# Kernel tuning notes

Hardware: AMD Instinct MI355X
Metric: run time of the kernel (lower is better)

Reference implementation:

```python
import jax, jax.numpy as jnp
import numpy as np

B, L, D, H = 2, 2048, 1024, 16
DK = D // H


def setup_inputs() -> dict:
    key = jax.random.key(0)
    ks = jax.random.split(key, 11)
    s = 0.02
    return {
        "q": jax.random.normal(ks[0], (B, L, D), jnp.float32),
        "k": jax.random.normal(ks[1], (B, L, D), jnp.float32),
        "v": jax.random.normal(ks[2], (B, L, D), jnp.float32),
        "mask": jnp.ones((B, 1, 1, L), jnp.int32),
        "wq": jax.random.normal(ks[3], (D, D), jnp.float32) * s,
        "bq": jnp.zeros((D,), jnp.float32),
        "wk": jax.random.normal(ks[4], (D, D), jnp.float32) * s,
        "bk": jnp.zeros((D,), jnp.float32),
        "wv": jax.random.normal(ks[5], (D, D), jnp.float32) * s,
        "bv": jnp.zeros((D,), jnp.float32),
        "wo": jax.random.normal(ks[6], (D, D), jnp.float32) * s,
        "bo": jnp.zeros((D,), jnp.float32),
    }


def _split_heads(x):
    # (B, L, D) -> (B, H, L, DK)
    return x.reshape(B, L, H, DK).transpose(0, 2, 1, 3)


def reference(q, k, v, mask, wq, bq, wk, bk, wv, bv, wo, bo):
    query = _split_heads(q @ wq.T + bq)
    key = _split_heads(k @ wk.T + bk)
    value = _split_heads(v @ wv.T + bv)
    scale = 1.0 / jnp.sqrt(jnp.asarray(DK, query.dtype))
    # (B, H, Lq, Lk) materialized scores, as in the original module
    scores = jnp.einsum('bhqd,bhkd->bhqk', query, key) * scale
    scores = jnp.where(mask == 0, jnp.asarray(-1e9, scores.dtype), scores)
    weights = jax.nn.softmax(scores, axis=-1)
    out = jnp.einsum('bhqk,bhkd->bhqd', weights, value)
    out = out.transpose(0, 2, 1, 3).reshape(B, L, D)
    return out @ wo.T + bo
```

## Files before the change

### kernel.cpp

```cpp
#include <hip/hip_runtime.h>
#include <hip/hip_bf16.h>


#define DEVINL __device__ __forceinline__

typedef __attribute__((ext_vector_type(8))) short short8;
typedef __attribute__((ext_vector_type(4))) float floatx4;

static constexpr int Bq = 2, Lq = 2048, Dm = 1024;
static constexpr int Mrows = Bq * Lq;
static constexpr size_t QKV_LD = 3072;
static constexpr int NT = Lq / 64;

DEVINL unsigned short f2bf(float x) {
  __hip_bfloat16 h = __float2bfloat16(x);
  unsigned short u;
  __builtin_memcpy(&u, &h, 2);
  return u;
}

DEVINL float bf2f(unsigned short u) {
  unsigned int t = ((unsigned int)u) << 16;
  float f;
  __builtin_memcpy(&f, &t, 4);
  return f;
}

DEVINL short8 cvt8(float4 a, float4 b) {
  union { unsigned short u[8]; short8 v; } o;
  o.u[0] = f2bf(a.x); o.u[1] = f2bf(a.y); o.u[2] = f2bf(a.z); o.u[3] = f2bf(a.w);
  o.u[4] = f2bf(b.x); o.u[5] = f2bf(b.y); o.u[6] = f2bf(b.z); o.u[7] = f2bf(b.w);
  return o.v;
}

DEVINL void gll16(const void* g, const void* l) {
  auto gp = (const __attribute__((address_space(1))) char*)(unsigned long long)(uintptr_t)g;
  auto lp = (__attribute__((address_space(3))) char*)(unsigned int)(uintptr_t)l;
  __builtin_amdgcn_global_load_lds(gp, lp, 16, 0, 0);
}

template <bool A_BF16, bool OUT_BF16>
__global__ __launch_bounds__(256) void gemm_k(
    const void* __restrict__ A0, const void* __restrict__ A1, const void* __restrict__ A2,
    const float* __restrict__ W0, const float* __restrict__ W1, const float* __restrict__ W2,
    const float* __restrict__ b0, const float* __restrict__ b1, const float* __restrict__ b2,
    void* __restrict__ Cout, int M, int N, int K, int ldc) {
  const int bid = blockIdx.x;
  const int xcd = bid & 7, sl = bid >> 3;
  const int g = xcd + ((sl >> 3) << 3), jn = sl & 7;
  const int z = g >> 5;
  const int m0 = (g & 31) * 128, n0 = jn * 128;

  const void* Aany = (z == 0) ? A0 : ((z == 1) ? A1 : A2);
  const float* W = (z == 0) ? W0 : ((z == 1) ? W1 : W2);
  const float* bias = (z == 0) ? b0 : ((z == 1) ? b1 : b2);
  const int tid = threadIdx.x, lane = tid & 63, w = tid >> 6;
  const int wr = w >> 1, wc = w & 1;

  __shared__ __align__(16) unsigned short As[2][128 * 32];
  __shared__ __align__(16) unsigned short Bs[2][128 * 32];

  floatx4 acc[4][4] = {};
  float4 wreg[2][2], areg[2][2];

  auto loadW = [&](int kt) {
#pragma unroll
    for (int it = 0; it < 2; ++it) {
      int gg = it * 256 + tid, row = gg >> 2, gk = gg & 3;
      const float* p = W + (size_t)(n0 + row) * K + kt + gk * 8;
      wreg[it][0] = ((const float4*)p)[0];
      wreg[it][1] = ((const float4*)p)[1];
    }
  };
  auto loadA = [&](int kt) {
#pragma unroll
    for (int it = 0; it < 2; ++it) {
      int gg = it * 256 + tid, row = gg >> 2, gk = gg & 3;
      const float* p = (const float*)Aany + (size_t)(m0 + row) * K + kt + gk * 8;
      areg[it][0] = ((const float4*)p)[0];
      areg[it][1] = ((const float4*)p)[1];
    }
  };
  auto writeW = [&](int buf) {
#pragma unroll
    for (int it = 0; it < 2; ++it) {
      int gg = it * 256 + tid, row = gg >> 2, gk = gg & 3;
      *(short8*)((char*)Bs + buf * 8192 + row * 64 + ((gk ^ (row & 3)) << 4)) =
          cvt8(wreg[it][0], wreg[it][1]);
    }
  };
  auto writeA = [&](int buf) {
#pragma unroll
    for (int it = 0; it < 2; ++it) {
      int gg = it * 256 + tid, row = gg >> 2, gk = gg & 3;
      *(short8*)((char*)As + buf * 8192 + row * 64 + ((gk ^ (row & 3)) << 4)) =
          cvt8(areg[it][0], areg[it][1]);
    }
  };
  auto stageA = [&](int kt, int buf) {
#pragma unroll
    for (int it = 0; it < 2; ++it) {
      int gg = it * 256 + tid, row = gg >> 2, gk = gg & 3;
      int koff = (gk ^ (row & 3)) * 8;
      gll16((const unsigned short*)Aany + (size_t)(m0 + row) * K + kt + koff,
            (const char*)As + buf * 8192 + (it * 256 + w * 64) * 16);
    }
  };

  const int nt = K / 32;
  loadW(0);
  if (!A_BF16) loadA(0);
  writeW(0);
  if (A_BF16) stageA(0, 0); else writeA(0);
  if (nt > 1) { loadW(32); if (!A_BF16) loadA(32); }
  __syncthreads();

  const int krow = lane >> 4;
  for (int t = 0; t < nt; ++t) {
    const int c = t & 1, n = c ^ 1;
    short8 af[4], bfr[4];
#pragma unroll
    for (int m = 0; m < 4; ++m) {
      int row = wr * 64 + m * 16 + (lane & 15);
      af[m] = *(const short8*)((const char*)As + c * 8192 + row * 64 + ((krow ^ (row & 3)) << 4));
    }
#pragma unroll
    for (int n2 = 0; n2 < 4; ++n2) {
      int row = wc * 64 + n2 * 16 + (lane & 15);
      bfr[n2] = *(const short8*)((const char*)Bs + c * 8192 + row * 64 + ((krow ^ (row & 3)) << 4));
    }
    if (t + 1 < nt) {
      writeW(n);
      if (A_BF16) stageA((t + 1) * 32, n); else writeA(n);
      if (t + 2 < nt) { loadW((t + 2) * 32); if (!A_BF16) loadA((t + 2) * 32); }
    }
    __builtin_amdgcn_s_setprio(1);
#pragma unroll
    for (int m = 0; m < 4; ++m)
#pragma unroll
      for (int n2 = 0; n2 < 4; ++n2)
        acc[m][n2] = __builtin_amdgcn_mfma_f32_16x16x32_bf16(af[m], bfr[n2], acc[m][n2], 0, 0, 0);
    __builtin_amdgcn_s_setprio(0);
    __syncthreads();
  }

  const int r4 = lane >> 4;
#pragma unroll
  for (int m = 0; m < 4; ++m)
#pragma unroll
    for (int n2 = 0; n2 < 4; ++n2) {
      int col = n0 + wc * 64 + n2 * 16 + (lane & 15);
      float bv = bias[col];
#pragma unroll
      for (int r = 0; r < 4; ++r) {
        int row = m0 + wr * 64 + m * 16 + r4 * 4 + r;
        float v = acc[m][n2][r] + bv;
        if (OUT_BF16)
          ((unsigned short*)Cout)[(size_t)row * ldc + (size_t)z * N + col] = f2bf(v);
        else
          ((float*)Cout)[(size_t)row * ldc + (size_t)z * N + col] = v;
      }
    }
}

__global__ __launch_bounds__(256) void attn_kernel(const unsigned short* __restrict__ QKV,
                                                   const int* __restrict__ mask,
                                                   unsigned short* __restrict__ Aout) {
  const int bid = blockIdx.x;
  const int xcd = bid & 7, sl = bid >> 3;
  const int bh = xcd + ((sl >> 5) << 3);
  const int q0 = (sl & 31) * 64;
  const int b = bh >> 4, h = bh & 15;
  const int tid = threadIdx.x, lane = tid & 63, w = tid >> 6;

  __shared__ __align__(16) unsigned short Klds[2][64 * 64];
  __shared__ __align__(16) unsigned short Vtlds[2][64 * 64];
  __shared__ __align__(16) unsigned short Plds[4][16 * 64];
  __shared__ int mflag[NT];

  const unsigned short* base = QKV + (size_t)b * Lq * QKV_LD;
  const unsigned short* Kbase = base + 1024;
  const unsigned short* Vbase = base + 2048;

  const int kp = tid & 31;
  const int vd0 = (tid >> 5) * 8;

  auto stageK = [&](int t, int buf) {
#pragma unroll
    for (int it = 0; it < 2; ++it) {
      int g = it * 256 + tid, key = g >> 3, gk = g & 7;
      gll16(Kbase + (size_t)(t * 64 + key) * QKV_LD + h * 64 + (gk ^ (key & 7)) * 8,
            (const char*)Klds + buf * 8192 + (it * 256 + w * 64) * 16);
    }
  };
  short8 vr0, vr1;
  auto loadV = [&](int t) {
    vr0 = *(const short8*)(Vbase + (size_t)(t * 64 + 2 * kp) * QKV_LD + h * 64 + vd0);
    vr1 = *(const short8*)(Vbase + (size_t)(t * 64 + 2 * kp + 1) * QKV_LD + h * 64 + vd0);
  };
  auto writeV = [&](int buf) {
#pragma unroll
    for (int i = 0; i < 8; ++i) {
      int d = vd0 + i;
      unsigned int val = (unsigned int)(unsigned short)vr0[i] |
                         ((unsigned int)(unsigned short)vr1[i] << 16);
      *(unsigned int*)((char*)Vtlds + buf * 8192 + d * 128 + (((kp >> 2) ^ (d & 7)) << 4) +
                       (kp & 3) * 4) = val;
    }
  };

  stageK(0, 0);
  loadV(0);
  writeV(0);
  {
    const int* mp = mask + b * Lq + tid * 8;
    int4 a = ((const int4*)mp)[0], bb = ((const int4*)mp)[1];
    int myall = (a.x && a.y && a.z && a.w && bb.x && bb.y && bb.z && bb.w) ? 1 : 0;
    unsigned long long bal = __ballot(myall);
    if (lane < 8) mflag[w * 8 + lane] = (((bal >> (lane * 8)) & 0xffull) == 0xffull);
  }

  short8 qf[2];
  {
    int row = q0 + w * 16 + (lane & 15);
#pragma unroll
    for (int c = 0; c < 2; ++c) {
      short8 raw = *(const short8*)(base + (size_t)row * QKV_LD + h * 64 + c * 32 + (lane >> 4) * 8);
      union { unsigned short u[8]; short8 v; } o2;
#pragma unroll
      for (int i = 0; i < 8; ++i) o2.u[i] = f2bf(bf2f((unsigned short)raw[i]) * 0.18033688f);
      qf[c] = o2.v;
    }
  }
  union { unsigned short u[8]; short8 v; } one_u;
#pragma unroll
  for (int i = 0; i < 8; ++i) one_u.u[i] = 0x3F80;
  const short8 ones8 = one_u.v;

  __syncthreads();

  floatx4 o[4] = {};
  floatx4 lacc = {};
  float mrow[4];
#pragma unroll
  for (int r = 0; r < 4; ++r) mrow[r] = -1e30f;

  for (int t = 0; t < NT; ++t) {
    const int c = t & 1, n = c ^ 1;
    if (t + 1 < NT) { stageK(t + 1, n); loadV(t + 1); }

    floatx4 s[4] = {};
    __builtin_amdgcn_s_setprio(1);
#pragma unroll
    for (int f = 0; f < 4; ++f) {
      int key = f * 16 + (lane & 15);
#pragma unroll
      for (int c2 = 0; c2 < 2; ++c2) {
        short8 kf = *(const short8*)((const char*)Klds + c * 8192 + key * 128 +
                                     (((c2 * 4 + (lane >> 4)) ^ (key & 7)) << 4));
        s[f] = __builtin_amdgcn_mfma_f32_16x16x32_bf16(qf[c2], kf, s[f], 0, 0, 0);
      }
    }
    __builtin_amdgcn_s_setprio(0);

    float tmax[4];
#pragma unroll
    for (int r = 0; r < 4; ++r)
      tmax[r] = fmaxf(fmaxf(s[0][r], s[1][r]), fmaxf(s[2][r], s[3][r]));
    const int allm = mflag[t];
    bool ok = (tmax[0] <= mrow[0] + 11.5f) && (tmax[1] <= mrow[1] + 11.5f) &&
              (tmax[2] <= mrow[2] + 11.5f) && (tmax[3] <= mrow[3] + 11.5f);
    if (__ballot(ok && allm) == ~0ull) {
#pragma unroll
      for (int f = 0; f < 4; ++f)
#pragma unroll
        for (int r = 0; r < 4; ++r) s[f][r] = __builtin_amdgcn_exp2f(s[f][r] - mrow[r]);
    } else {
#pragma unroll
      for (int dx = 1; dx <= 8; dx <<= 1)
#pragma unroll
        for (int r = 0; r < 4; ++r) tmax[r] = fmaxf(tmax[r], __shfl_xor(tmax[r], dx, 64));
      float mnew[4], alpha[4];
#pragma unroll
      for (int r = 0; r < 4; ++r) {
        mnew[r] = fmaxf(mrow[r], tmax[r]);
        alpha[r] = __builtin_amdgcn_exp2f(mrow[r] - mnew[r]);
        mrow[r] = mnew[r];
      }
#pragma unroll
      for (int df = 0; df < 4; ++df)
#pragma unroll
        for (int r = 0; r < 4; ++r) o[df][r] *= alpha[r];
#pragma unroll
      for (int r = 0; r < 4; ++r) lacc[r] *= alpha[r];
      if (allm) {
#pragma unroll
        for (int f = 0; f < 4; ++f)
#pragma unroll
          for (int r = 0; r < 4; ++r) s[f][r] = __builtin_amdgcn_exp2f(s[f][r] - mnew[r]);
      } else {
#pragma unroll
        for (int f = 0; f < 4; ++f) {
          int mv = mask[b * Lq + t * 64 + f * 16 + (lane & 15)];
#pragma unroll
          for (int r = 0; r < 4; ++r)
            s[f][r] = mv ? __builtin_amdgcn_exp2f(s[f][r] - mnew[r]) : 0.f;
        }
      }
    }

#pragma unroll
    for (int f = 0; f < 4; ++f)
#pragma unroll
      for (int r = 0; r < 4; ++r) {
        int row = (lane >> 4) * 4 + r, col = f * 16 + (lane & 15);
        *(unsigned short*)((char*)&Plds[w][0] + row * 128 + (((col >> 3) ^ (row & 7)) << 4) +
                           (col & 7) * 2) = f2bf(s[f][r]);
      }

    short8 pf[2];
#pragma unroll
    for (int kc = 0; kc < 2; ++kc)
      pf[kc] = *(const short8*)((const char*)&Plds[w][0] + (lane & 15) * 128 +
                                (((kc * 4 + (lane >> 4)) ^ (lane & 7)) << 4));
    __builtin_amdgcn_s_setprio(1);
    lacc = __builtin_amdgcn_mfma_f32_16x16x32_bf16(pf[0], ones8, lacc, 0, 0, 0);
    lacc = __builtin_amdgcn_mfma_f32_16x16x32_bf16(pf[1], ones8, lacc, 0, 0, 0);
#pragma unroll
    for (int df = 0; df < 4; ++df) {
      int d = df * 16 + (lane & 15);
#pragma unroll
      for (int kc = 0; kc < 2; ++kc) {
        short8 vf = *(const short8*)((const char*)Vtlds + c * 8192 + d * 128 +
                                     (((kc * 4 + (lane >> 4)) ^ (d & 7)) << 4));
        o[df] = __builtin_amdgcn_mfma_f32_16x16x32_bf16(pf[kc], vf, o[df], 0, 0, 0);
      }
    }
    __builtin_amdgcn_s_setprio(0);

    if (t + 1 < NT) writeV(n);
    __syncthreads();
  }

  float rl[4];
#pragma unroll
  for (int r = 0; r < 4; ++r) rl[r] = 1.0f / lacc[r];
#pragma unroll
  for (int df = 0; df < 4; ++df)
#pragma unroll
    for (int r = 0; r < 4; ++r) {
      int row = q0 + w * 16 + (lane >> 4) * 4 + r;
      int col = h * 64 + df * 16 + (lane & 15);
      Aout[(size_t)(b * Lq + row) * Dm + col] = f2bf(o[df][r] * rl[r]);
    }
}

extern "C" void kernel_launch(void* const* d_in, const int* in_sizes, int n_in,
                              void* d_out, int out_size, void* d_ws, size_t ws_size,
                              hipStream_t stream) {
  const float* q = (const float*)d_in[0];
  const float* k = (const float*)d_in[1];
  const float* v = (const float*)d_in[2];
  const int* maskp = (const int*)d_in[3];
  const float* wq = (const float*)d_in[4];
  const float* bq = (const float*)d_in[5];
  const float* wk = (const float*)d_in[6];
  const float* bk = (const float*)d_in[7];
  const float* wv = (const float*)d_in[8];
  const float* bv = (const float*)d_in[9];
  const float* wo = (const float*)d_in[10];
  const float* bo = (const float*)d_in[11];

  unsigned short* qkv = (unsigned short*)d_ws;
  unsigned short* attnout = qkv + (size_t)Mrows * QKV_LD;

  gemm_k<false, true><<<dim3(768), 256, 0, stream>>>(
      q, k, v, wq, wk, wv, bq, bk, bv, qkv, Mrows, Dm, Dm, (int)QKV_LD);

  attn_kernel<<<dim3(1024), 256, 0, stream>>>(qkv, maskp, attnout);

  gemm_k<true, false><<<dim3(256), 256, 0, stream>>>(
      attnout, attnout, attnout, wo, wo, wo, bo, bo, bo, d_out, Mrows, Dm, Dm, Dm);
}
```

Measured before the change: 278.3 us.

## Pre-cast weights to bf16, stage them via direct LDS loads, widen attention blocks

Adds small cast kernels that convert the QKV and output projection weights to bf16 once per call, storing them in scratch space in the output buffer and workspace. The GEMM then stages W tiles into LDS with global_load_lds instead of loading fp32 into registers, converting, and writing to LDS. The GEMM block-to-tile mapping is also changed per launch. The attention kernel moves to 512-thread blocks covering 128 queries, so each staged K/V tile is reused by twice as many waves. The cost is two extra kernel launches and extra weight traffic, and the attention blocks use more LDS and registers.

```diff
diff --git a/kernel.cpp b/kernel.cpp
--- a/kernel.cpp
+++ b/kernel.cpp
@@ -11,6 +11,7 @@
 static constexpr int Mrows = Bq * Lq;
 static constexpr size_t QKV_LD = 3072;
 static constexpr int NT = Lq / 64;
+static constexpr size_t NW = (size_t)Dm * Dm;
 
 DEVINL unsigned short f2bf(float x) {
   __hip_bfloat16 h = __float2bfloat16(x);
@@ -39,20 +40,41 @@
   __builtin_amdgcn_global_load_lds(gp, lp, 16, 0, 0);
 }
 
+__global__ __launch_bounds__(256) void castw(const float* __restrict__ w0,
+                                             const float* __restrict__ w1,
+                                             const float* __restrict__ w2,
+                                             unsigned short* __restrict__ dst) {
+  const int z = blockIdx.y;
+  const float* s = (z == 0) ? w0 : ((z == 1) ? w1 : w2);
+  int i = blockIdx.x * 256 + threadIdx.x;
+  float4 a = ((const float4*)s)[i * 2];
+  float4 b = ((const float4*)s)[i * 2 + 1];
+  ((short8*)(dst + (size_t)z * NW))[i] = cvt8(a, b);
+}
+
+__global__ __launch_bounds__(256) void castw1(const float* __restrict__ s,
+                                              unsigned short* __restrict__ dst) {
+  int i = blockIdx.x * 256 + threadIdx.x;
+  float4 a = ((const float4*)s)[i * 2];
+  float4 b = ((const float4*)s)[i * 2 + 1];
+  ((short8*)dst)[i] = cvt8(a, b);
+}
+
 template <bool A_BF16, bool OUT_BF16>
 __global__ __launch_bounds__(256) void gemm_k(
     const void* __restrict__ A0, const void* __restrict__ A1, const void* __restrict__ A2,
-    const float* __restrict__ W0, const float* __restrict__ W1, const float* __restrict__ W2,
+    const unsigned short* __restrict__ Wb,
     const float* __restrict__ b0, const float* __restrict__ b1, const float* __restrict__ b2,
-    void* __restrict__ Cout, int M, int N, int K, int ldc) {
+    void* __restrict__ Cout, int M, int N, int K, int ldc, int GPX) {
   const int bid = blockIdx.x;
-  const int xcd = bid & 7, sl = bid >> 3;
-  const int g = xcd + ((sl >> 3) << 3), jn = sl & 7;
-  const int z = g >> 5;
-  const int m0 = (g & 31) * 128, n0 = jn * 128;
+  const int xcd = bid & 7, rest = bid >> 3;
+  const int qg = rest >> 3, jn = rest & 7;
+  const int G = xcd * GPX + qg;
+  const int z = G >> 5;
+  const int m0 = (G & 31) * 128, n0 = jn * 128;
 
   const void* Aany = (z == 0) ? A0 : ((z == 1) ? A1 : A2);
-  const float* W = (z == 0) ? W0 : ((z == 1) ? W1 : W2);
+  const unsigned short* W = Wb + (size_t)z * N * K;
   const float* bias = (z == 0) ? b0 : ((z == 1) ? b1 : b2);
   const int tid = threadIdx.x, lane = tid & 63, w = tid >> 6;
   const int wr = w >> 1, wc = w & 1;
@@ -61,15 +83,24 @@
   __shared__ __align__(16) unsigned short Bs[2][128 * 32];
 
   floatx4 acc[4][4] = {};
-  float4 wreg[2][2], areg[2][2];
-
-  auto loadW = [&](int kt) {
+  float4 areg[2][2];
+
+  auto stageW = [&](int kt, int buf) {
 #pragma unroll
     for (int it = 0; it < 2; ++it) {
       int gg = it * 256 + tid, row = gg >> 2, gk = gg & 3;
-      const float* p = W + (size_t)(n0 + row) * K + kt + gk * 8;
-      wreg[it][0] = ((const float4*)p)[0];
-      wreg[it][1] = ((const float4*)p)[1];
+      int koff = (gk ^ (row & 3)) * 8;
+      gll16(W + (size_t)(n0 + row) * K + kt + koff,
+            (const char*)Bs + buf * 8192 + (it * 256 + w * 64) * 16);
+    }
+  };
+  auto stageA = [&](int kt, int buf) {
+#pragma unroll
+    for (int it = 0; it < 2; ++it) {
+      int gg = it * 256 + tid, row = gg >> 2, gk = gg & 3;
+      int koff = (gk ^ (row & 3)) * 8;
+      gll16((const unsigned short*)Aany + (size_t)(m0 + row) * K + kt + koff,
+            (const char*)As + buf * 8192 + (it * 256 + w * 64) * 16);
     }
   };
   auto loadA = [&](int kt) {
@@ -81,14 +112,6 @@
       areg[it][1] = ((const float4*)p)[1];
     }
   };
-  auto writeW = [&](int buf) {
-#pragma unroll
-    for (int it = 0; it < 2; ++it) {
-      int gg = it * 256 + tid, row = gg >> 2, gk = gg & 3;
-      *(short8*)((char*)Bs + buf * 8192 + row * 64 + ((gk ^ (row & 3)) << 4)) =
-          cvt8(wreg[it][0], wreg[it][1]);
-    }
-  };
   auto writeA = [&](int buf) {
 #pragma unroll
     for (int it = 0; it < 2; ++it) {
@@ -97,27 +120,26 @@
           cvt8(areg[it][0], areg[it][1]);
     }
   };
-  auto stageA = [&](int kt, int buf) {
-#pragma unroll
-    for (int it = 0; it < 2; ++it) {
-      int gg = it * 256 + tid, row = gg >> 2, gk = gg & 3;
-      int koff = (gk ^ (row & 3)) * 8;
-      gll16((const unsigned short*)Aany + (size_t)(m0 + row) * K + kt + koff,
-            (const char*)As + buf * 8192 + (it * 256 + w * 64) * 16);
-    }
-  };
 
   const int nt = K / 32;
-  loadW(0);
   if (!A_BF16) loadA(0);
-  writeW(0);
+  stageW(0, 0);
   if (A_BF16) stageA(0, 0); else writeA(0);
-  if (nt > 1) { loadW(32); if (!A_BF16) loadA(32); }
+  if (!A_BF16 && nt > 1) loadA(32);
   __syncthreads();
 
   const int krow = lane >> 4;
   for (int t = 0; t < nt; ++t) {
     const int c = t & 1, n = c ^ 1;
+    if (t + 1 < nt) {
+      stageW((t + 1) * 32, n);
+      if (A_BF16) {
+        stageA((t + 1) * 32, n);
+      } else {
+        writeA(n);
+        if (t + 2 < nt) loadA((t + 2) * 32);
+      }
+    }
     short8 af[4], bfr[4];
 #pragma unroll
     for (int m = 0; m < 4; ++m) {
@@ -128,11 +150,6 @@
     for (int n2 = 0; n2 < 4; ++n2) {
       int row = wc * 64 + n2 * 16 + (lane & 15);
       bfr[n2] = *(const short8*)((const char*)Bs + c * 8192 + row * 64 + ((krow ^ (row & 3)) << 4));
-    }
-    if (t + 1 < nt) {
-      writeW(n);
-      if (A_BF16) stageA((t + 1) * 32, n); else writeA(n);
-      if (t + 2 < nt) { loadW((t + 2) * 32); if (!A_BF16) loadA((t + 2) * 32); }
     }
     __builtin_amdgcn_s_setprio(1);
 #pragma unroll
@@ -163,19 +180,19 @@
     }
 }
 
-__global__ __launch_bounds__(256) void attn_kernel(const unsigned short* __restrict__ QKV,
+__global__ __launch_bounds__(512) void attn_kernel(const unsigned short* __restrict__ QKV,
                                                    const int* __restrict__ mask,
                                                    unsigned short* __restrict__ Aout) {
   const int bid = blockIdx.x;
   const int xcd = bid & 7, sl = bid >> 3;
-  const int bh = xcd + ((sl >> 5) << 3);
-  const int q0 = (sl & 31) * 64;
+  const int bh = xcd + ((sl >> 4) << 3);
+  const int q0 = (sl & 15) * 128;
   const int b = bh >> 4, h = bh & 15;
   const int tid = threadIdx.x, lane = tid & 63, w = tid >> 6;
 
   __shared__ __align__(16) unsigned short Klds[2][64 * 64];
   __shared__ __align__(16) unsigned short Vtlds[2][64 * 64];
-  __shared__ __align__(16) unsigned short Plds[4][16 * 64];
+  __shared__ __align__(16) unsigned short Plds[8][16 * 64];
   __shared__ int mflag[NT];
 
   const unsigned short* base = QKV + (size_t)b * Lq * QKV_LD;
@@ -183,15 +200,12 @@
   const unsigned short* Vbase = base + 2048;
 
   const int kp = tid & 31;
-  const int vd0 = (tid >> 5) * 8;
+  const int vd0 = ((tid >> 5) & 7) * 8;
 
   auto stageK = [&](int t, int buf) {
-#pragma unroll
-    for (int it = 0; it < 2; ++it) {
-      int g = it * 256 + tid, key = g >> 3, gk = g & 7;
-      gll16(Kbase + (size_t)(t * 64 + key) * QKV_LD + h * 64 + (gk ^ (key & 7)) * 8,
-            (const char*)Klds + buf * 8192 + (it * 256 + w * 64) * 16);
-    }
+    int key = tid >> 3, gk = tid & 7;
+    gll16(Kbase + (size_t)(t * 64 + key) * QKV_LD + h * 64 + (gk ^ (key & 7)) * 8,
+          (const char*)Klds + buf * 8192 + w * 1024);
   };
   short8 vr0, vr1;
   auto loadV = [&](int t) {
@@ -210,9 +224,9 @@
   };
 
   stageK(0, 0);
-  loadV(0);
-  writeV(0);
-  {
+  if (tid < 256) {
+    loadV(0);
+    writeV(0);
     const int* mp = mask + b * Lq + tid * 8;
     int4 a = ((const int4*)mp)[0], bb = ((const int4*)mp)[1];
     int myall = (a.x && a.y && a.z && a.w && bb.x && bb.y && bb.z && bb.w) ? 1 : 0;
@@ -247,7 +261,10 @@
 
   for (int t = 0; t < NT; ++t) {
     const int c = t & 1, n = c ^ 1;
-    if (t + 1 < NT) { stageK(t + 1, n); loadV(t + 1); }
+    if (t + 1 < NT) {
+      stageK(t + 1, n);
+      if (tid < 256) loadV(t + 1);
+    }
 
     floatx4 s[4] = {};
     __builtin_amdgcn_s_setprio(1);
@@ -338,7 +355,7 @@
     }
     __builtin_amdgcn_s_setprio(0);
 
-    if (t + 1 < NT) writeV(n);
+    if (t + 1 < NT && tid < 256) writeV(n);
     __syncthreads();
   }
 
@@ -371,14 +388,20 @@
   const float* wo = (const float*)d_in[10];
   const float* bo = (const float*)d_in[11];
 
-  unsigned short* qkv = (unsigned short*)d_ws;
-  unsigned short* attnout = qkv + (size_t)Mrows * QKV_LD;
+  unsigned short* wqkv_bf = (unsigned short*)d_out;
+  unsigned short* attnout = (unsigned short*)d_ws;
+  unsigned short* qkv = attnout + (size_t)Mrows * Dm;
+  unsigned short* wo_bf = qkv;
+
+  castw<<<dim3(NW / 8 / 256, 3), 256, 0, stream>>>(wq, wk, wv, wqkv_bf);
 
   gemm_k<false, true><<<dim3(768), 256, 0, stream>>>(
-      q, k, v, wq, wk, wv, bq, bk, bv, qkv, Mrows, Dm, Dm, (int)QKV_LD);
-
-  attn_kernel<<<dim3(1024), 256, 0, stream>>>(qkv, maskp, attnout);
+      q, k, v, wqkv_bf, bq, bk, bv, qkv, Mrows, Dm, Dm, (int)QKV_LD, 12);
+
+  attn_kernel<<<dim3(512), 512, 0, stream>>>(qkv, maskp, attnout);
+
+  castw1<<<dim3(NW / 8 / 256), 256, 0, stream>>>(wo, wo_bf);
 
   gemm_k<true, false><<<dim3(256), 256, 0, stream>>>(
-      attnout, attnout, attnout, wo, wo, wo, bo, bo, bo, d_out, Mrows, Dm, Dm, Dm);
-}
+      attnout, attnout, attnout, wo_bf, bo, bo, bo, d_out, Mrows, Dm, Dm, Dm, 4);
+}
```

New measurement: 255.7 us. 1.09x faster.
